# Performance work log

Measured on AMD Instinct MI355X. Metric: run time of the kernel, lower is better.

The kernel has to match this reference:

```python
import jax, jax.numpy as jnp
import numpy as np

N, T = 64, 256
TOTAL_NODES, C_IN = 25, 128          # c = 3200
NUM_SEEDS, C_OUT = 5, 3              # seeds flat dim = 15
NEW_NODES = 20
LIN_IN = TOTAL_NODES * C_IN + NUM_SEEDS * C_OUT  # 3215


def setup_inputs() -> dict:
    key = jax.random.key(0)
    k1, k2, k3 = jax.random.split(key, 3)
    x = jax.random.normal(k1, (N, T, TOTAL_NODES * C_IN), dtype=jnp.float32)
    seeds = jax.random.normal(k2, (N, T, NUM_SEEDS, C_OUT), dtype=jnp.float32)
    # Stacked weights of the `new_nodes` cloned Linear(LIN_IN, C_OUT) layers.
    W = jax.random.normal(k3, (NEW_NODES, C_OUT, LIN_IN), dtype=jnp.float32) * 0.02
    b = jnp.zeros((NEW_NODES, C_OUT), dtype=jnp.float32)
    return {"x": x, "seeds": seeds, "W": W, "b": b}


def reference(x, seeds, W, b):
    n, t, _ = x.shape
    mix = jnp.concatenate([x, seeds.reshape(n, t, -1)], axis=2)  # [n,t,LIN_IN]
    # Fuse all cloned small Linears into one batched GEMM, then layout as
    # torch.stack([...], dim=3): output [n, t, c_out, new_nodes].
    out = jnp.einsum('ntc,koc->ntok', mix, W) + b.T  # b.T: [c_out, new_nodes]
    return out
```

## Files before the change

kernel.cpp:

```cpp
#include <hip/hip_runtime.h>


#define NROWS    16384
#define CIN      3200
#define SEED_K   15
#define LIN_IN   3215
#define NCOL     60
#define KB_MAIN  100
#define KB_TOT   101
#define WB_ELEMS (KB_TOT * 4 * 64 * 8)

typedef __attribute__((ext_vector_type(8))) __bf16 bf16x8;
typedef __attribute__((ext_vector_type(4))) float f32x4;
typedef __attribute__((ext_vector_type(8))) unsigned short ushort8;

__device__ inline unsigned short f2bf_rne(float f) {
    unsigned int u = __builtin_bit_cast(unsigned int, f);
    u += 0x7fffu + ((u >> 16) & 1u);
    return (unsigned short)(u >> 16);
}

__device__ inline bf16x8 to_bf16x8(f32x4 a0, f32x4 a1) {
    ushort8 u;
    u[0] = f2bf_rne(a0[0]); u[1] = f2bf_rne(a0[1]);
    u[2] = f2bf_rne(a0[2]); u[3] = f2bf_rne(a0[3]);
    u[4] = f2bf_rne(a1[0]); u[5] = f2bf_rne(a1[1]);
    u[6] = f2bf_rne(a1[2]); u[7] = f2bf_rne(a1[3]);
    return __builtin_bit_cast(bf16x8, u);
}

__global__ void prep_B(const float* __restrict__ W, unsigned short* __restrict__ Wb) {
    int idx = blockIdx.x * blockDim.x + threadIdx.x;
    if (idx >= WB_ELEMS) return;
    int jj   = idx & 7;
    int lane = (idx >> 3) & 63;
    int nt   = (idx >> 9) & 3;
    int kb   = idx >> 11;
    int k = kb * 32 + (lane >> 4) * 8 + jj;
    int n = nt * 16 + (lane & 15);
    float v = 0.0f;
    if (k < LIN_IN && n < NCOL) {
        int o = n / 20, kn = n % 20;
        v = W[(kn * 3 + o) * LIN_IN + k];
    }
    Wb[idx] = f2bf_rne(v);
}

__global__ __launch_bounds__(256) void gen_nodes_gemm(
    const float* __restrict__ x, const float* __restrict__ seeds,
    const float* __restrict__ b, const unsigned short* __restrict__ Wb,
    float* __restrict__ out) {
    const int lane = threadIdx.x & 63;
    const int wave = threadIdx.x >> 6;
    const int quad = lane >> 4;
    const int l15  = lane & 15;
    const int row_base = blockIdx.x * 64 + wave * 16;
    const int arow = row_base + l15;

    const float* xrow = x + (size_t)arow * CIN + quad * 8;

    f32x4 acc[4];
#pragma unroll
    for (int i = 0; i < 4; ++i) acc[i] = (f32x4){0.f, 0.f, 0.f, 0.f};

#pragma unroll 4
    for (int kb = 0; kb < KB_MAIN; ++kb) {
        const f32x4* ap = (const f32x4*)(xrow + kb * 32);
        f32x4 a0 = ap[0];
        f32x4 a1 = ap[1];
        const unsigned short* bb = Wb + (size_t)kb * 2048 + lane * 8;
        bf16x8 b0 = *(const bf16x8*)(bb);
        bf16x8 b1 = *(const bf16x8*)(bb + 512);
        bf16x8 b2 = *(const bf16x8*)(bb + 1024);
        bf16x8 b3 = *(const bf16x8*)(bb + 1536);
        bf16x8 af = to_bf16x8(a0, a1);
        acc[0] = __builtin_amdgcn_mfma_f32_16x16x32_bf16(af, b0, acc[0], 0, 0, 0);
        acc[1] = __builtin_amdgcn_mfma_f32_16x16x32_bf16(af, b1, acc[1], 0, 0, 0);
        acc[2] = __builtin_amdgcn_mfma_f32_16x16x32_bf16(af, b2, acc[2], 0, 0, 0);
        acc[3] = __builtin_amdgcn_mfma_f32_16x16x32_bf16(af, b3, acc[3], 0, 0, 0);
    }

    {
        const float* srow = seeds + (size_t)arow * SEED_K;
        f32x4 s0 = {0.f, 0.f, 0.f, 0.f}, s1 = {0.f, 0.f, 0.f, 0.f};
#pragma unroll
        for (int j = 0; j < 4; ++j) {
            int c = quad * 8 + j;
            if (c < SEED_K) s0[j] = srow[c];
            if (c + 4 < SEED_K) s1[j] = srow[c + 4];
        }
        bf16x8 af = to_bf16x8(s0, s1);
        const unsigned short* bb = Wb + (size_t)KB_MAIN * 2048 + lane * 8;
        bf16x8 b0 = *(const bf16x8*)(bb);
        bf16x8 b1 = *(const bf16x8*)(bb + 512);
        bf16x8 b2 = *(const bf16x8*)(bb + 1024);
        bf16x8 b3 = *(const bf16x8*)(bb + 1536);
        acc[0] = __builtin_amdgcn_mfma_f32_16x16x32_bf16(af, b0, acc[0], 0, 0, 0);
        acc[1] = __builtin_amdgcn_mfma_f32_16x16x32_bf16(af, b1, acc[1], 0, 0, 0);
        acc[2] = __builtin_amdgcn_mfma_f32_16x16x32_bf16(af, b2, acc[2], 0, 0, 0);
        acc[3] = __builtin_amdgcn_mfma_f32_16x16x32_bf16(af, b3, acc[3], 0, 0, 0);
    }

#pragma unroll
    for (int nt = 0; nt < 4; ++nt) {
        int j = nt * 16 + l15;
        if (j < NCOL) {
            float bias = b[(j % 20) * 3 + (j / 20)];
#pragma unroll
            for (int r = 0; r < 4; ++r) {
                int m = quad * 4 + r;
                out[(size_t)(row_base + m) * NCOL + j] = acc[nt][r] + bias;
            }
        }
    }
}

extern "C" void kernel_launch(void* const* d_in, const int* in_sizes, int n_in,
                              void* d_out, int out_size, void* d_ws, size_t ws_size,
                              hipStream_t stream) {
    const float* x     = (const float*)d_in[0];
    const float* seeds = (const float*)d_in[1];
    const float* W     = (const float*)d_in[2];
    const float* b     = (const float*)d_in[3];
    float* out = (float*)d_out;
    unsigned short* Wb = (unsigned short*)d_ws;

    prep_B<<<(WB_ELEMS + 255) / 256, 256, 0, stream>>>(W, Wb);
    gen_nodes_gemm<<<NROWS / 64, 256, 0, stream>>>(x, seeds, b, Wb, out);
}
```

Measured before the change: 308.5 us.

## Split K across four waves per 16-row tile with LDS reduction

Each block now handles 16 rows instead of 64, and its four waves each process a quarter of the K dimension. The partial accumulators are summed through shared memory by wave 0, which adds the bias and writes the output. This launches four times as many blocks to raise memory-level parallelism for the bandwidth-bound x stream. The cost is an LDS reduction and a barrier per block. The bf16 weight buffer also moves from the workspace into a device global array.

```diff
diff --git a/kernel.cpp b/kernel.cpp
--- a/kernel.cpp
+++ b/kernel.cpp
@@ -8,11 +8,14 @@
 #define NCOL     60
 #define KB_MAIN  100
 #define KB_TOT   101
+#define KB_CHUNK 25
 #define WB_ELEMS (KB_TOT * 4 * 64 * 8)
 
 typedef __attribute__((ext_vector_type(8))) __bf16 bf16x8;
 typedef __attribute__((ext_vector_type(4))) float f32x4;
 typedef __attribute__((ext_vector_type(8))) unsigned short ushort8;
+
+__device__ unsigned short Wb_g[WB_ELEMS];
 
 __device__ inline unsigned short f2bf_rne(float f) {
     unsigned int u = __builtin_bit_cast(unsigned int, f);
@@ -29,7 +32,7 @@
     return __builtin_bit_cast(bf16x8, u);
 }
 
-__global__ void prep_B(const float* __restrict__ W, unsigned short* __restrict__ Wb) {
+__global__ void prep_B(const float* __restrict__ W) {
     int idx = blockIdx.x * blockDim.x + threadIdx.x;
     if (idx >= WB_ELEMS) return;
     int jj   = idx & 7;
@@ -43,18 +46,17 @@
         int o = n / 20, kn = n % 20;
         v = W[(kn * 3 + o) * LIN_IN + k];
     }
-    Wb[idx] = f2bf_rne(v);
+    Wb_g[idx] = f2bf_rne(v);
 }
 
-__global__ __launch_bounds__(256) void gen_nodes_gemm(
+__global__ __launch_bounds__(256, 4) void gen_nodes_gemm(
     const float* __restrict__ x, const float* __restrict__ seeds,
-    const float* __restrict__ b, const unsigned short* __restrict__ Wb,
-    float* __restrict__ out) {
+    const float* __restrict__ b, float* __restrict__ out) {
     const int lane = threadIdx.x & 63;
     const int wave = threadIdx.x >> 6;
     const int quad = lane >> 4;
     const int l15  = lane & 15;
-    const int row_base = blockIdx.x * 64 + wave * 16;
+    const int row_base = blockIdx.x * 16;
     const int arow = row_base + l15;
 
     const float* xrow = x + (size_t)arow * CIN + quad * 8;
@@ -63,12 +65,15 @@
 #pragma unroll
     for (int i = 0; i < 4; ++i) acc[i] = (f32x4){0.f, 0.f, 0.f, 0.f};
 
-#pragma unroll 4
-    for (int kb = 0; kb < KB_MAIN; ++kb) {
+    const int kb0 = wave * KB_CHUNK;
+    const int kb1 = kb0 + KB_CHUNK;
+
+#pragma unroll 2
+    for (int kb = kb0; kb < kb1; ++kb) {
         const f32x4* ap = (const f32x4*)(xrow + kb * 32);
         f32x4 a0 = ap[0];
         f32x4 a1 = ap[1];
-        const unsigned short* bb = Wb + (size_t)kb * 2048 + lane * 8;
+        const unsigned short* bb = Wb_g + (size_t)kb * 2048 + lane * 8;
         bf16x8 b0 = *(const bf16x8*)(bb);
         bf16x8 b1 = *(const bf16x8*)(bb + 512);
         bf16x8 b2 = *(const bf16x8*)(bb + 1024);
@@ -80,7 +85,7 @@
         acc[3] = __builtin_amdgcn_mfma_f32_16x16x32_bf16(af, b3, acc[3], 0, 0, 0);
     }
 
-    {
+    if (wave == 3) {
         const float* srow = seeds + (size_t)arow * SEED_K;
         f32x4 s0 = {0.f, 0.f, 0.f, 0.f}, s1 = {0.f, 0.f, 0.f, 0.f};
 #pragma unroll
@@ -90,7 +95,7 @@
             if (c + 4 < SEED_K) s1[j] = srow[c + 4];
         }
         bf16x8 af = to_bf16x8(s0, s1);
-        const unsigned short* bb = Wb + (size_t)KB_MAIN * 2048 + lane * 8;
+        const unsigned short* bb = Wb_g + (size_t)KB_MAIN * 2048 + lane * 8;
         bf16x8 b0 = *(const bf16x8*)(bb);
         bf16x8 b1 = *(const bf16x8*)(bb + 512);
         bf16x8 b2 = *(const bf16x8*)(bb + 1024);
@@ -101,15 +106,29 @@
         acc[3] = __builtin_amdgcn_mfma_f32_16x16x32_bf16(af, b3, acc[3], 0, 0, 0);
     }
 
+    __shared__ float red[3][16][68];
+    if (wave != 0) {
 #pragma unroll
-    for (int nt = 0; nt < 4; ++nt) {
-        int j = nt * 16 + l15;
-        if (j < NCOL) {
-            float bias = b[(j % 20) * 3 + (j / 20)];
+        for (int nt = 0; nt < 4; ++nt)
 #pragma unroll
-            for (int r = 0; r < 4; ++r) {
-                int m = quad * 4 + r;
-                out[(size_t)(row_base + m) * NCOL + j] = acc[nt][r] + bias;
+            for (int r = 0; r < 4; ++r)
+                red[wave - 1][quad * 4 + r][nt * 16 + l15] = acc[nt][r];
+    }
+    __syncthreads();
+
+    if (wave == 0) {
+#pragma unroll
+        for (int nt = 0; nt < 4; ++nt) {
+            int j = nt * 16 + l15;
+            if (j < NCOL) {
+                float bias = b[(j % 20) * 3 + (j / 20)];
+#pragma unroll
+                for (int r = 0; r < 4; ++r) {
+                    int m = quad * 4 + r;
+                    float v = acc[nt][r] + red[0][m][j] + red[1][m][j]
+                            + red[2][m][j] + bias;
+                    out[(size_t)(row_base + m) * NCOL + j] = v;
+                }
             }
         }
     }
@@ -123,8 +142,8 @@
     const float* W     = (const float*)d_in[2];
     const float* b     = (const float*)d_in[3];
     float* out = (float*)d_out;
-    unsigned short* Wb = (unsigned short*)d_ws;
+    (void)d_ws; (void)ws_size;
 
-    prep_B<<<(WB_ELEMS + 255) / 256, 256, 0, stream>>>(W, Wb);
-    gen_nodes_gemm<<<NROWS / 64, 256, 0, stream>>>(x, seeds, b, Wb, out);
+    prep_B<<<(WB_ELEMS + 255) / 256, 256, 0, stream>>>(W);
+    gen_nodes_gemm<<<NROWS / 16, 256, 0, stream>>>(x, seeds, b, out);
 }
```

Result: no change. 306.8 us (-0.5%).

## Stage A and B tiles through LDS with async double-buffered global_load_lds

Applied to the files above, without the earlier changes.

Replaces direct per-wave global loads with a double-buffered LDS pipeline filled by global_load_lds. Two waves stage the x tiles and two stage the bf16 weight tiles, and each block now covers 32 rows with the N dimension split across waves. Weights and bias move to device-global buffers, and the bias gather is precomputed. The goal is to overlap memory fetch with MFMA work and share B tiles, at the cost of a __syncthreads per chunk and twice as many blocks.

```diff
diff --git a/kernel.cpp b/kernel.cpp
--- a/kernel.cpp
+++ b/kernel.cpp
@@ -9,10 +9,18 @@
 #define KB_MAIN  100
 #define KB_TOT   101
 #define WB_ELEMS (KB_TOT * 4 * 64 * 8)
+#define CHUNK_KB 2
+#define NCHUNKS  50
+#define A_BYTES  1024
+#define B_BASE   16384
+#define SMEM_SZ  32768
 
 typedef __attribute__((ext_vector_type(8))) __bf16 bf16x8;
 typedef __attribute__((ext_vector_type(4))) float f32x4;
 typedef __attribute__((ext_vector_type(8))) unsigned short ushort8;
+
+__device__ unsigned short Wb_g[WB_ELEMS];
+__device__ __align__(16) float bias_g[64];
 
 __device__ inline unsigned short f2bf_rne(float f) {
     unsigned int u = __builtin_bit_cast(unsigned int, f);
@@ -25,13 +33,20 @@
     u[0] = f2bf_rne(a0[0]); u[1] = f2bf_rne(a0[1]);
     u[2] = f2bf_rne(a0[2]); u[3] = f2bf_rne(a0[3]);
     u[4] = f2bf_rne(a1[0]); u[5] = f2bf_rne(a1[1]);
-    u[6] = f2bf_rne(a1[2]); u[7] = f2bf_rne(a1[3]);
+    u[6] = f2bf_rne(a1[2]); u[7] = f2bf_rne(a1[2 + 1]);
     return __builtin_bit_cast(bf16x8, u);
 }
 
-__global__ void prep_B(const float* __restrict__ W, unsigned short* __restrict__ Wb) {
+typedef __attribute__((address_space(3))) void lds_void;
+typedef __attribute__((address_space(1))) const void gm_void;
+__device__ __forceinline__ void gll16(const void* g, void* l) {
+    __builtin_amdgcn_global_load_lds((gm_void*)g, (lds_void*)l, 16, 0, 0);
+}
+
+__global__ void prep_B(const float* __restrict__ W, const float* __restrict__ b) {
     int idx = blockIdx.x * blockDim.x + threadIdx.x;
     if (idx >= WB_ELEMS) return;
+    if (idx < 64) bias_g[idx] = (idx < NCOL) ? b[(idx % 20) * 3 + (idx / 20)] : 0.f;
     int jj   = idx & 7;
     int lane = (idx >> 3) & 63;
     int nt   = (idx >> 9) & 3;
@@ -43,73 +58,98 @@
         int o = n / 20, kn = n % 20;
         v = W[(kn * 3 + o) * LIN_IN + k];
     }
-    Wb[idx] = f2bf_rne(v);
+    Wb_g[idx] = f2bf_rne(v);
 }
 
-__global__ __launch_bounds__(256) void gen_nodes_gemm(
+__global__ __launch_bounds__(256) void gen_nodes(
     const float* __restrict__ x, const float* __restrict__ seeds,
-    const float* __restrict__ b, const unsigned short* __restrict__ Wb,
     float* __restrict__ out) {
     const int lane = threadIdx.x & 63;
     const int wave = threadIdx.x >> 6;
     const int quad = lane >> 4;
     const int l15  = lane & 15;
-    const int row_base = blockIdx.x * 64 + wave * 16;
-    const int arow = row_base + l15;
+    const int rb0  = blockIdx.x * 32;
+    const int wt   = wave & 1;
+    const int nh   = wave >> 1;
 
-    const float* xrow = x + (size_t)arow * CIN + quad * 8;
+    __shared__ __align__(16) char smem[SMEM_SZ];
 
-    f32x4 acc[4];
+    const float* xlane = x + (size_t)(rb0 + l15) * CIN + quad * 8;
+
+    f32x4 acc[2];
+    acc[0] = (f32x4){0.f, 0.f, 0.f, 0.f};
+    acc[1] = (f32x4){0.f, 0.f, 0.f, 0.f};
+
+    auto stage = [&](int c, int buf) {
+        if (wave < 2) {
+            const int kb  = wave;
+            const int cbk = c * CHUNK_KB + kb;
+            const float* s0 = xlane + (size_t)cbk * 32;
+            char* ab = smem + ((buf * 2 + kb) * 4) * A_BYTES;
+            gll16(s0,                ab);
+            gll16(s0 + 4,            ab + 1024);
+            gll16(s0 + 16 * CIN,     ab + 2048);
+            gll16(s0 + 16 * CIN + 4, ab + 3072);
+        } else {
+            const int kb  = wave - 2;
+            const int cbk = c * CHUNK_KB + kb;
+            const unsigned short* s = Wb_g + (size_t)cbk * 2048 + lane * 8;
+            char* bb = smem + B_BASE + ((buf * 2 + kb) * 4) * A_BYTES;
+            gll16(s,        bb);
+            gll16(s + 512,  bb + 1024);
+            gll16(s + 1024, bb + 2048);
+            gll16(s + 1536, bb + 3072);
+        }
+    };
+
+    stage(0, 0);
+    __syncthreads();
+
+    for (int c = 0; c < NCHUNKS; ++c) {
+        const int buf = c & 1;
+        if (c + 1 < NCHUNKS) stage(c + 1, buf ^ 1);
+
 #pragma unroll
-    for (int i = 0; i < 4; ++i) acc[i] = (f32x4){0.f, 0.f, 0.f, 0.f};
-
-#pragma unroll 4
-    for (int kb = 0; kb < KB_MAIN; ++kb) {
-        const f32x4* ap = (const f32x4*)(xrow + kb * 32);
-        f32x4 a0 = ap[0];
-        f32x4 a1 = ap[1];
-        const unsigned short* bb = Wb + (size_t)kb * 2048 + lane * 8;
-        bf16x8 b0 = *(const bf16x8*)(bb);
-        bf16x8 b1 = *(const bf16x8*)(bb + 512);
-        bf16x8 b2 = *(const bf16x8*)(bb + 1024);
-        bf16x8 b3 = *(const bf16x8*)(bb + 1536);
-        bf16x8 af = to_bf16x8(a0, a1);
-        acc[0] = __builtin_amdgcn_mfma_f32_16x16x32_bf16(af, b0, acc[0], 0, 0, 0);
-        acc[1] = __builtin_amdgcn_mfma_f32_16x16x32_bf16(af, b1, acc[1], 0, 0, 0);
-        acc[2] = __builtin_amdgcn_mfma_f32_16x16x32_bf16(af, b2, acc[2], 0, 0, 0);
-        acc[3] = __builtin_amdgcn_mfma_f32_16x16x32_bf16(af, b3, acc[3], 0, 0, 0);
+        for (int kb = 0; kb < CHUNK_KB; ++kb) {
+            const char* ab = smem + (((buf * 2 + kb) * 2 + wt) * 2) * A_BYTES + lane * 16;
+            f32x4 a0 = *(const f32x4*)(ab);
+            f32x4 a1 = *(const f32x4*)(ab + 1024);
+            const char* bb = smem + B_BASE + ((buf * 2 + kb) * 4 + nh * 2) * A_BYTES + lane * 16;
+            bf16x8 b0 = *(const bf16x8*)(bb);
+            bf16x8 b1 = *(const bf16x8*)(bb + 1024);
+            bf16x8 af = to_bf16x8(a0, a1);
+            acc[0] = __builtin_amdgcn_mfma_f32_16x16x32_bf16(af, b0, acc[0], 0, 0, 0);
+            acc[1] = __builtin_amdgcn_mfma_f32_16x16x32_bf16(af, b1, acc[1], 0, 0, 0);
+        }
+        __syncthreads();
     }
 
     {
-        const float* srow = seeds + (size_t)arow * SEED_K;
+        const float* srow = seeds + (size_t)(rb0 + wt * 16 + l15) * SEED_K;
         f32x4 s0 = {0.f, 0.f, 0.f, 0.f}, s1 = {0.f, 0.f, 0.f, 0.f};
 #pragma unroll
         for (int j = 0; j < 4; ++j) {
-            int c = quad * 8 + j;
-            if (c < SEED_K) s0[j] = srow[c];
-            if (c + 4 < SEED_K) s1[j] = srow[c + 4];
+            int cc = quad * 8 + j;
+            if (cc < SEED_K) s0[j] = srow[cc];
+            if (cc + 4 < SEED_K) s1[j] = srow[cc + 4];
         }
         bf16x8 af = to_bf16x8(s0, s1);
-        const unsigned short* bb = Wb + (size_t)KB_MAIN * 2048 + lane * 8;
-        bf16x8 b0 = *(const bf16x8*)(bb);
-        bf16x8 b1 = *(const bf16x8*)(bb + 512);
-        bf16x8 b2 = *(const bf16x8*)(bb + 1024);
-        bf16x8 b3 = *(const bf16x8*)(bb + 1536);
+        const unsigned short* bb = Wb_g + (size_t)KB_MAIN * 2048 + lane * 8;
+        bf16x8 b0 = *(const bf16x8*)(bb + nh * 1024);
+        bf16x8 b1 = *(const bf16x8*)(bb + nh * 1024 + 512);
         acc[0] = __builtin_amdgcn_mfma_f32_16x16x32_bf16(af, b0, acc[0], 0, 0, 0);
         acc[1] = __builtin_amdgcn_mfma_f32_16x16x32_bf16(af, b1, acc[1], 0, 0, 0);
-        acc[2] = __builtin_amdgcn_mfma_f32_16x16x32_bf16(af, b2, acc[2], 0, 0, 0);
-        acc[3] = __builtin_amdgcn_mfma_f32_16x16x32_bf16(af, b3, acc[3], 0, 0, 0);
     }
 
 #pragma unroll
-    for (int nt = 0; nt < 4; ++nt) {
-        int j = nt * 16 + l15;
+    for (int t = 0; t < 2; ++t) {
+        int j = (nh * 2 + t) * 16 + l15;
         if (j < NCOL) {
-            float bias = b[(j % 20) * 3 + (j / 20)];
+            float bias = bias_g[j];
 #pragma unroll
             for (int r = 0; r < 4; ++r) {
-                int m = quad * 4 + r;
-                out[(size_t)(row_base + m) * NCOL + j] = acc[nt][r] + bias;
+                int m = wt * 16 + quad * 4 + r;
+                out[(size_t)(rb0 + m) * NCOL + j] = acc[t][r] + bias;
             }
         }
     }
@@ -123,8 +163,8 @@
     const float* W     = (const float*)d_in[2];
     const float* b     = (const float*)d_in[3];
     float* out = (float*)d_out;
-    unsigned short* Wb = (unsigned short*)d_ws;
+    (void)d_ws; (void)ws_size;
 
-    prep_B<<<(WB_ELEMS + 255) / 256, 256, 0, stream>>>(W, Wb);
-    gen_nodes_gemm<<<NROWS / 64, 256, 0, stream>>>(x, seeds, b, Wb, out);
+    prep_B<<<(WB_ELEMS + 255) / 256, 256, 0, stream>>>(W, b);
+    gen_nodes<<<NROWS / 32, 256, 0, stream>>>(x, seeds, out);
 }
```

Result: faster. 298.0 us (-3.4%).
